# Performance work log

Measured on AMD Instinct MI355X. Metric: run time of the kernel, lower is better.

## Reference

```python
import jax, jax.numpy as jnp
import numpy as np

B, N, F, E = 4, 256, 128, 128
HID = 128      # link ConvLSTM hidden channels
L_PROP = 2     # propagate_layers
SUB, AFF = 10, 12


def setup_inputs() -> dict:
    key = jax.random.key(0)
    ks = jax.random.split(key, 16)
    s = 0.02
    inp = dict(
        edge_features=jax.random.normal(ks[0], (B, E, N, N), jnp.float32),
        node_features=jax.random.normal(ks[1], (B, F, N), jnp.float32),
        adj_mat=jax.random.uniform(ks[2], (B, N, N), dtype=jnp.float32),
        node_labels=jnp.zeros((B, N, AFF), jnp.float32),
        args=0,
    )
    # GraphConvLSTM link function: two 1x1-conv LSTM cells + 1x1 output conv
    inp['W_lstm0'] = s * jax.random.normal(ks[3], (4 * HID, E + HID), jnp.float32)
    inp['b_lstm0'] = jnp.zeros((4 * HID,), jnp.float32)
    inp['W_lstm1'] = s * jax.random.normal(ks[4], (4 * HID, HID + HID), jnp.float32)
    inp['b_lstm1'] = jnp.zeros((4 * HID,), jnp.float32)
    inp['W_link_out'] = s * jax.random.normal(ks[5], (1, HID), jnp.float32)
    inp['b_link_out'] = jnp.zeros((1,), jnp.float32)
    # linear_concat message: Linear(2F+E -> E)
    inp['W_msg'] = s * jax.random.normal(ks[6], (E, 2 * F + E), jnp.float32)
    inp['b_msg'] = jnp.zeros((E,), jnp.float32)
    # two GRU update functions (node 0 vs other nodes), input E, hidden F
    inp['Wih0'] = s * jax.random.normal(ks[7], (3 * F, E), jnp.float32)
    inp['Whh0'] = s * jax.random.normal(ks[8], (3 * F, F), jnp.float32)
    inp['bih0'] = jnp.zeros((3 * F,), jnp.float32)
    inp['bhh0'] = jnp.zeros((3 * F,), jnp.float32)
    inp['Wih1'] = s * jax.random.normal(ks[9], (3 * F, E), jnp.float32)
    inp['Whh1'] = s * jax.random.normal(ks[10], (3 * F, F), jnp.float32)
    inp['bih1'] = jnp.zeros((3 * F,), jnp.float32)
    inp['bhh1'] = jnp.zeros((3 * F,), jnp.float32)
    # fc_soft_max readouts
    inp['Wr0'] = s * jax.random.normal(ks[11], (SUB, F), jnp.float32)
    inp['br0'] = jnp.zeros((SUB,), jnp.float32)
    inp['Wr1'] = s * jax.random.normal(ks[12], (AFF, F), jnp.float32)
    inp['br1'] = jnp.zeros((AFF,), jnp.float32)
    return inp


def _link_fun(he, Ws, bs, Wo, bo):
    # he: [B, C, N, N] edge states -> predicted soft adjacency [B, N, N]
    x = he
    for W, b in zip(Ws, bs):
        hid = W.shape[0] // 4
        h0 = jnp.zeros(x.shape[:1] + (hid,) + x.shape[2:], x.dtype)
        xc = jnp.concatenate([x, h0], axis=1)
        g = jnp.einsum('oc,bcvw->bovw', W, xc) + b[None, :, None, None]
        i_g, f_g, g_g, o_g = jnp.split(g, 4, axis=1)
        c = jax.nn.sigmoid(i_g) * jnp.tanh(g_g)  # forget*c0 vanishes (c0=0)
        x = jax.nn.sigmoid(o_g) * jnp.tanh(c)
    a = jnp.einsum('oc,bcvw->bovw', Wo, x) + bo[None, :, None, None]
    return jax.nn.sigmoid(a)[:, 0]  # [B, N, N]


def _messages(node_features, edge_features, A, W_msg, b_msg):
    # X[b,:,w,i] = concat(h_i, h_w, e[i,w]); m[b,o,w,i] = (W_msg X + b) * A[b,i,w]
    hv = jnp.broadcast_to(node_features[:, :, None, :], (B, F, N, N))
    hw = jnp.broadcast_to(node_features[:, :, :, None], (B, F, N, N))
    ev = jnp.swapaxes(edge_features, 2, 3)
    X = jnp.concatenate([hv, hw, ev], axis=1)  # [B, 2F+E, N, N]
    m = jnp.einsum('of,bfwi->bowi', W_msg, X) + b_msg[None, :, None, None]
    return m * jnp.swapaxes(A, 1, 2)[:, None, :, :]


def _gru(x, h, Wih, Whh, bih, bhh):
    gi = x @ Wih.T + bih
    gh = h @ Whh.T + bhh
    ir, iz, inn = jnp.split(gi, 3, axis=-1)
    hr, hz, hn = jnp.split(gh, 3, axis=-1)
    r = jax.nn.sigmoid(ir + hr)
    z = jax.nn.sigmoid(iz + hz)
    n = jnp.tanh(inn + r * hn)
    return (1.0 - z) * n + z * h


def reference(edge_features, node_features, adj_mat, node_labels, args,
              W_lstm0, b_lstm0, W_lstm1, b_lstm1, W_link_out, b_link_out,
              W_msg, b_msg, Wih0, Whh0, bih0, bhh0, Wih1, Whh1, bih1, bhh1,
              Wr0, br0, Wr1, br1):
    he = edge_features  # hidden_edge_states[0]
    A = None
    m_sum = None
    for _ in range(L_PROP):
        A = _link_fun(he, [W_lstm0, W_lstm1], [b_lstm0, b_lstm1], W_link_out, b_link_out)
        m = _messages(node_features, edge_features, A, W_msg, b_msg)
        he = m                     # hidden_edge_states[r+1][:,:,:,i] = m_v
        m_sum = m.sum(axis=2)      # [B, E, N]: sum over source nodes w
    # GRU update (hidden node states are never rewritten in the source, so
    # only the last round's update feeds the readout)
    h = jnp.swapaxes(node_features, 1, 2)  # [B, N, F]
    x = jnp.swapaxes(m_sum, 1, 2)          # [B, N, E]
    h_new0 = _gru(x[:, :1], h[:, :1], Wih0, Whh0, bih0, bhh0)  # node 0
    h_new1 = _gru(x[:, 1:], h[:, 1:], Wih1, Whh1, bih1, bhh1)  # other nodes
    out0 = jax.nn.log_softmax(h_new0[:, 0] @ Wr0.T + br0, axis=-1)  # [B, SUB]
    out1 = jax.nn.log_softmax(h_new1 @ Wr1.T + br1, axis=-1)        # [B, N-1, AFF]
    pred = jnp.zeros(node_labels.shape, node_labels.dtype)
    pred = pred.at[:, 0, :SUB].set(out0)
    pred = pred.at[:, 1:, :].set(out1)
    return A, pred
```

## Files before the change

kernel.cpp:

```cpp
#include <hip/hip_runtime.h>

#define CH 128
#define PIXTOT (4*256*256)
#define L2E 1.4426950408889634f

typedef unsigned short u16;
typedef short short8 __attribute__((ext_vector_type(8)));
typedef float f32x4 __attribute__((ext_vector_type(4)));

__device__ __forceinline__ float bf2f(u16 u){ return __uint_as_float(((unsigned)u)<<16); }
__device__ __forceinline__ u16 f2bf(float f){
  return (u16)((__float_as_uint(f) + 0x8000u) >> 16);
}
__device__ __forceinline__ float fexp2(float x){ return __builtin_amdgcn_exp2f(x); }
__device__ __forceinline__ float frcp(float x){ return __builtin_amdgcn_rcpf(x); }
__device__ __forceinline__ float sigm(float x){ return frcp(1.f + fexp2(-L2E*x)); }
__device__ __forceinline__ float tanh_f(float x){ return 1.f - 2.f*frcp(fexp2(2.f*L2E*x)+1.f); }

__global__ __launch_bounds__(256) void wcvt_kernel(
    const float* __restrict__ W0, const float* __restrict__ bl0,
    const float* __restrict__ W1, const float* __restrict__ bl1,
    const float* __restrict__ Wm,
    u16* __restrict__ W0c, u16* __restrict__ W1c,
    float* __restrict__ b0c, float* __restrict__ b1c,
    u16* __restrict__ Wmc)
{
  int idx = blockIdx.x*256 + threadIdx.x;
  int row = idx >> 7, col = idx & 127;
  int slot = row >> 7;
  int src = (row < 128) ? row : row + 128;
  float s = (slot == 1) ? (2.f*L2E) : (-L2E);
  W0c[idx] = f2bf(W0[(size_t)src*256 + col] * s);
  W1c[idx] = f2bf(W1[(size_t)src*256 + col] * s);
  if (idx < 16384)
    Wmc[idx] = f2bf(Wm[(size_t)(idx>>7)*384 + 256 + (idx&127)]);
  if (idx < 384){
    b0c[idx] = bl0[src] * s;
    b1c[idx] = bl1[src] * s;
  }
}

__global__ __launch_bounds__(128) void uv_kernel(
    const float* __restrict__ nf, const float* __restrict__ Wmsg,
    const float* __restrict__ bmsg, float* __restrict__ U, float* __restrict__ V)
{
  int blk = blockIdx.x; int b = blk >> 8; int i = blk & 255;
  __shared__ float xs[128];
  int t = threadIdx.x;
  xs[t] = nf[((size_t)(b*CH + t))*256 + i];
  __syncthreads();
  float su = bmsg[t];
  float sv = 0.f;
  const float* w1 = Wmsg + (size_t)t*384;
  const float* w2 = w1 + 128;
  for (int f=0; f<128; f++){ float xf = xs[f]; su += w1[f]*xf; sv += w2[f]*xf; }
  U[((size_t)(b*256 + i))*CH + t] = su;
  V[((size_t)(b*256 + i))*CH + t] = sv;
}

__device__ __forceinline__ void stage_edge(
    const float* __restrict__ edge, int b, int q1, int w0, u16 (*xs)[136], int t)
{
  const int c = t >> 1, ph = (t & 1) * 32;
  const float* src = edge + ((size_t)(b*CH + c)*256 + q1)*256 + w0 + ph;
  #pragma unroll
  for (int j=0; j<8; j++){
    f32x4 v = *(const f32x4*)(src + j*4);
    u16* dst = &xs[ph + j*4][c];
    dst[0*136]=f2bf(v[0]); dst[1*136]=f2bf(v[1]);
    dst[2*136]=f2bf(v[2]); dst[3*136]=f2bf(v[3]);
  }
}

template<bool LAST>
__device__ __forceinline__ void lstm_layer(
    const u16 (*xin)[136], u16 (*xout)[136],
    const u16* __restrict__ W, const float* __restrict__ Bc,
    int oc0, int lm, int quad, const float woc[2][4], float* partial)
{
  f32x4 acc[3][2][4];
  #pragma unroll
  for (int g=0; g<3; g++)
    #pragma unroll
    for (int rs=0; rs<2; rs++)
      #pragma unroll
      for (int nt=0; nt<4; nt++){ f32x4 z = {0.f,0.f,0.f,0.f}; acc[g][rs][nt] = z; }
  #pragma unroll
  for (int k0=0; k0<128; k0+=32){
    short8 bfr[4];
    #pragma unroll
    for (int nt=0; nt<4; nt++)
      bfr[nt] = *(const short8*)&xin[nt*16+lm][k0 + quad*8];
    #pragma unroll
    for (int g=0; g<3; g++){
      #pragma unroll
      for (int rs=0; rs<2; rs++){
        const short8 afr = *(const short8*)(W + ((size_t)(g*128 + oc0 + rs*16 + lm))*128 + k0 + quad*8);
        #pragma unroll
        for (int nt=0; nt<4; nt++)
          acc[g][rs][nt] = __builtin_amdgcn_mfma_f32_16x16x32_bf16(afr, bfr[nt], acc[g][rs][nt], 0, 0, 0);
      }
    }
  }
  #pragma unroll
  for (int rs=0; rs<2; rs++){
    float bi[3][4];
    #pragma unroll
    for (int g=0; g<3; g++)
      #pragma unroll
      for (int r=0; r<4; r++) bi[g][r] = Bc[g*128 + oc0 + rs*16 + quad*4 + r];
    #pragma unroll
    for (int nt=0; nt<4; nt++){
      ushort4 w4;
      #pragma unroll
      for (int r=0; r<4; r++){
        float iv = acc[0][rs][nt][r] + bi[0][r];
        float gv = fminf(acc[1][rs][nt][r] + bi[1][r], 80.f);
        float ov = acc[2][rs][nt][r] + bi[2][r];
        float a  = fexp2(iv);
        float bb = fexp2(gv);
        float f  = fexp2(ov);
        float c  = (bb - 1.f) * frcp((1.f + a) * (bb + 1.f));
        float c2 = c*c, c4 = c2*c2;
        float p  = __builtin_fmaf(c2, 105.f, 945.f) + c4;
        float q  = __builtin_fmaf(c4, 15.f, __builtin_fmaf(c2, 420.f, 945.f));
        float xo = c * p * frcp(q * (1.f + f));
        if (LAST) partial[nt] = __builtin_fmaf(xo, woc[rs][r], partial[nt]);
        else      ((u16*)&w4)[r] = f2bf(xo);
      }
      if (!LAST)
        *(ushort4*)&xout[nt*16+lm][oc0 + rs*16 + quad*4] = w4;
    }
  }
}

template<int MODE>
__global__ __launch_bounds__(256, 2) void link_kernel(
    const float* __restrict__ edge, const float* __restrict__ A1,
    const float* __restrict__ U, const float* __restrict__ V,
    const u16* __restrict__ Wmc,
    const u16* __restrict__ W0c, const float* __restrict__ B0c,
    const u16* __restrict__ W1c, const float* __restrict__ B1c,
    const float* __restrict__ Wo, const float* __restrict__ Bo,
    float* __restrict__ Aout, float* __restrict__ outA, float* __restrict__ A2nat)
{
  __shared__ u16 xs[64][136];
  __shared__ u16 ys[64][136];
  __shared__ float red[64][17];
  const int t = threadIdx.x;
  const int Q0 = blockIdx.x * 64;
  const int b = Q0 >> 16, q1 = (Q0 >> 8) & 255, w0 = Q0 & 255;
  stage_edge(edge, b, q1, w0, xs, t);
  const int wv = t >> 6, lane = t & 63, lm = lane & 15, quad = lane >> 4;
  const int oc0 = wv*32;
  float woc[2][4];
  #pragma unroll
  for (int rs=0; rs<2; rs++){
    const f32x4 wv4 = *(const f32x4*)(Wo + oc0 + rs*16 + quad*4);
    #pragma unroll
    for (int r=0; r<4; r++) woc[rs][r] = wv4[r];
  }
  __syncthreads();
  if (MODE){
    f32x4 acc[2][4];
    #pragma unroll
    for (int rs=0; rs<2; rs++)
      #pragma unroll
      for (int nt=0; nt<4; nt++){ f32x4 z = {0.f,0.f,0.f,0.f}; acc[rs][nt] = z; }
    #pragma unroll
    for (int k0=0; k0<128; k0+=32){
      short8 bfr[4];
      #pragma unroll
      for (int nt=0; nt<4; nt++)
        bfr[nt] = *(const short8*)&xs[nt*16+lm][k0 + quad*8];
      #pragma unroll
      for (int rs=0; rs<2; rs++){
        const short8 afr = *(const short8*)(Wmc + ((size_t)(oc0 + rs*16 + lm))*128 + k0 + quad*8);
        #pragma unroll
        for (int nt=0; nt<4; nt++)
          acc[rs][nt] = __builtin_amdgcn_mfma_f32_16x16x32_bf16(afr, bfr[nt], acc[rs][nt], 0, 0, 0);
      }
    }
    #pragma unroll
    for (int rs=0; rs<2; rs++){
      const int o0 = oc0 + rs*16 + quad*4;
      const f32x4 ug = *(const f32x4*)(U + ((size_t)(b*256 + q1))*CH + o0);
      #pragma unroll
      for (int nt=0; nt<4; nt++){
        const int px = nt*16 + lm;
        const float a1 = A1[Q0 + px];
        const f32x4 vg = *(const f32x4*)(V + ((size_t)(b*256 + w0 + px))*CH + o0);
        ushort4 w4;
        #pragma unroll
        for (int r=0; r<4; r++)
          ((u16*)&w4)[r] = f2bf((acc[rs][nt][r] + ug[r] + vg[r]) * a1);
        *(ushort4*)&ys[px][o0] = w4;
      }
    }
    __syncthreads();
  }
  const u16 (*in0)[136] = MODE ? (const u16(*)[136])ys : (const u16(*)[136])xs;
  u16 (*buf)[136] = MODE ? xs : ys;
  float partial[4] = {0.f, 0.f, 0.f, 0.f};
  lstm_layer<false>(in0, buf, W0c, B0c, oc0, lm, quad, woc, partial);
  __syncthreads();
  lstm_layer<true>((const u16(*)[136])buf, (u16(*)[136])nullptr, W1c, B1c, oc0, lm, quad, woc, partial);
  #pragma unroll
  for (int nt=0; nt<4; nt++) red[nt*16+lm][wv*4+quad] = partial[nt];
  __syncthreads();
  if (t < 64){
    float s = Bo[0];
    #pragma unroll
    for (int k=0; k<16; k++) s += red[t][k];
    const float sg = sigm(s);
    Aout[Q0 + t] = sg;
    if (MODE){
      const size_t p = (size_t)b*65536 + (size_t)(w0 + t)*256 + q1;
      outA[p]  = sg;
      A2nat[p] = sg;
    }
  }
}

__global__ __launch_bounds__(256) void se_kernel(
    const float* __restrict__ edge, const float* __restrict__ A2nat,
    float* __restrict__ s_e, float* __restrict__ sA)
{
  const int b = blockIdx.x >> 8, i = blockIdx.x & 255;
  __shared__ float al[256];
  __shared__ float sb[2][128];
  __shared__ float rr[64];
  const int t = threadIdx.x;
  al[t] = A2nat[((size_t)(b*256 + i))*256 + t];
  __syncthreads();
  const int c = t & 127, half = t >> 7;
  const float* src = edge + (((size_t)(b*CH + c))*256 + i)*256 + half*128;
  float s = 0.f;
  #pragma unroll
  for (int j=0; j<32; j++){
    const f32x4 v = *(const f32x4*)(src + j*4);
    const float* ap = &al[half*128 + j*4];
    s += v[0]*ap[0] + v[1]*ap[1] + v[2]*ap[2] + v[3]*ap[3];
  }
  sb[half][c] = s;
  if (t < 64) rr[t] = al[t] + al[t+64] + al[t+128] + al[t+192];
  __syncthreads();
  if (t < 128) s_e[((size_t)(b*256 + i))*CH + t] = sb[0][t] + sb[1][t];
  if (t == 0){
    float sa = 0.f;
    for (int k=0; k<64; k++) sa += rr[k];
    sA[b*256 + i] = sa;
  }
}

__global__ __launch_bounds__(128) void mfinal_kernel(
    const float* __restrict__ s_e, const float* __restrict__ sA,
    const float* __restrict__ A2nat, const float* __restrict__ V,
    const float* __restrict__ Wmsg, const float* __restrict__ U,
    float* __restrict__ msum)
{
  const int b = blockIdx.x >> 8, i = blockIdx.x & 255;
  __shared__ float se_s[128];
  __shared__ float al[256];
  const int t = threadIdx.x;
  se_s[t] = s_e[((size_t)(b*256 + i))*CH + t];
  al[t]       = A2nat[((size_t)(b*256 + i))*256 + t];
  al[t + 128] = A2nat[((size_t)(b*256 + i))*256 + t + 128];
  __syncthreads();
  const float* w3 = Wmsg + (size_t)t*384 + 256;
  float s = U[((size_t)(b*256 + i))*CH + t] * sA[b*256 + i];
  #pragma unroll 4
  for (int k=0; k<128; k+=4){
    const f32x4 wv4 = *(const f32x4*)(w3 + k);
    s += wv4[0]*se_s[k] + wv4[1]*se_s[k+1] + wv4[2]*se_s[k+2] + wv4[3]*se_s[k+3];
  }
  const float* vp = V + ((size_t)(b*256))*CH + t;
  #pragma unroll 8
  for (int w=0; w<256; w++)
    s += al[w] * vp[(size_t)w*CH];
  msum[((size_t)(b*256 + i))*CH + t] = s;
}

__global__ __launch_bounds__(128) void k5_kernel(
    const float* __restrict__ msum, const float* __restrict__ nf,
    const float* __restrict__ Wih0, const float* __restrict__ Whh0,
    const float* __restrict__ bih0, const float* __restrict__ bhh0,
    const float* __restrict__ Wih1, const float* __restrict__ Whh1,
    const float* __restrict__ bih1, const float* __restrict__ bhh1,
    const float* __restrict__ Wr0, const float* __restrict__ br0,
    const float* __restrict__ Wr1, const float* __restrict__ br1,
    float* __restrict__ outp)
{
  const int blk = blockIdx.x, b = blk >> 8, n = blk & 255;
  __shared__ float xsh[128], hsh[128], hnew[128], lg[16];
  const int t = threadIdx.x;
  xsh[t] = msum[((size_t)(b*256 + n))*CH + t];
  hsh[t] = nf[((size_t)(b*CH + t))*256 + n];
  __syncthreads();
  const float* Wih = n ? Wih1 : Wih0;  const float* Whh = n ? Whh1 : Whh0;
  const float* bih = n ? bih1 : bih0;  const float* bhh = n ? bhh1 : bhh0;
  float gi[3], gh[3];
  #pragma unroll
  for (int prt=0; prt<3; prt++){
    int row = prt*128 + t;
    const float* wi_ = Wih + (size_t)row*CH;
    const float* wh_ = Whh + (size_t)row*CH;
    float si = 0.f, sh2 = 0.f;
    for (int k=0; k<128; k+=4){
      f32x4 wv1 = *(const f32x4*)(wi_ + k);
      f32x4 wv2 = *(const f32x4*)(wh_ + k);
      #pragma unroll
      for (int j=0; j<4; j++){ si += wv1[j]*xsh[k+j]; sh2 += wv2[j]*hsh[k+j]; }
    }
    gi[prt] = si + bih[row];
    gh[prt] = sh2 + bhh[row];
  }
  float r  = sigm(gi[0] + gh[0]);
  float z  = sigm(gi[1] + gh[1]);
  float ng = tanh_f(gi[2] + r*gh[2]);
  hnew[t] = (1.f - z)*ng + z*hsh[t];
  __syncthreads();
  const int K = n ? 12 : 10;
  const float* Wr = n ? Wr1 : Wr0;  const float* br = n ? br1 : br0;
  if (t < K){
    const float* wr_ = Wr + (size_t)t*CH;
    float s = 0.f;
    for (int k=0; k<128; k+=4){
      f32x4 wv1 = *(const f32x4*)(wr_ + k);
      #pragma unroll
      for (int j=0; j<4; j++) s += wv1[j]*hnew[k+j];
    }
    lg[t] = s + br[t];
  }
  __syncthreads();
  if (t < 12){
    float o = 0.f;
    if (t < K){
      float mx = -1e30f;
      for (int j=0; j<K; j++) mx = fmaxf(mx, lg[j]);
      float se = 0.f;
      for (int j=0; j<K; j++) se += __expf(lg[j] - mx);
      o = lg[t] - mx - __logf(se);
    }
    outp[((size_t)(b*256 + n))*12 + t] = o;
  }
}

extern "C" void kernel_launch(void* const* d_in, const int* in_sizes, int n_in,
                              void* d_out, int out_size, void* d_ws, size_t ws_size,
                              hipStream_t stream)
{
  (void)in_sizes; (void)n_in; (void)out_size; (void)ws_size;
  const float* edge = (const float*)d_in[0];
  const float* nf   = (const float*)d_in[1];
  const float* Wl0  = (const float*)d_in[5];
  const float* bl0  = (const float*)d_in[6];
  const float* Wl1  = (const float*)d_in[7];
  const float* bl1  = (const float*)d_in[8];
  const float* Wlo  = (const float*)d_in[9];
  const float* blo  = (const float*)d_in[10];
  const float* Wmsg = (const float*)d_in[11];
  const float* bmsg = (const float*)d_in[12];
  const float* Wih0 = (const float*)d_in[13];
  const float* Whh0 = (const float*)d_in[14];
  const float* bih0 = (const float*)d_in[15];
  const float* bhh0 = (const float*)d_in[16];
  const float* Wih1 = (const float*)d_in[17];
  const float* Whh1 = (const float*)d_in[18];
  const float* bih1 = (const float*)d_in[19];
  const float* bhh1 = (const float*)d_in[20];
  const float* Wr0  = (const float*)d_in[21];
  const float* br0  = (const float*)d_in[22];
  const float* Wr1  = (const float*)d_in[23];
  const float* br1  = (const float*)d_in[24];

  char* ws = (char*)d_ws;
  float* A1v   = (float*)(ws);
  float* A2nat = (float*)(ws + 1048576);
  float* U     = (float*)(ws + 2097152);
  float* V     = (float*)(ws + 2621440);
  float* msum  = (float*)(ws + 3145728);
  float* s_e   = (float*)(ws + 3670016);
  float* sAr   = (float*)(ws + 4194304);
  u16*   W0c   = (u16*)(ws + 4198400);
  u16*   W1c   = (u16*)(ws + 4296704);
  u16*   Wmc   = (u16*)(ws + 4395008);
  float* b0c   = (float*)(ws + 4427776);
  float* b1c   = (float*)(ws + 4429312);

  float* outA = (float*)d_out;
  float* outP = outA + (size_t)PIXTOT;

  wcvt_kernel<<<dim3(192), dim3(256), 0, stream>>>(
      Wl0, bl0, Wl1, bl1, Wmsg, W0c, W1c, b0c, b1c, Wmc);
  uv_kernel<<<dim3(4*256), dim3(128), 0, stream>>>(nf, Wmsg, bmsg, U, V);
  link_kernel<0><<<dim3(PIXTOT/64), dim3(256), 0, stream>>>(
      edge, (const float*)nullptr, U, V, Wmc, W0c, b0c, W1c, b1c, Wlo, blo,
      A1v, (float*)nullptr, (float*)nullptr);
  link_kernel<1><<<dim3(PIXTOT/64), dim3(256), 0, stream>>>(
      edge, A1v, U, V, Wmc, W0c, b0c, W1c, b1c, Wlo, blo,
      A1v, outA, A2nat);
  se_kernel<<<dim3(4*256), dim3(256), 0, stream>>>(edge, A2nat, s_e, sAr);
  mfinal_kernel<<<dim3(4*256), dim3(128), 0, stream>>>(
      s_e, sAr, A2nat, V, Wmsg, U, msum);
  k5_kernel<<<dim3(4*256), dim3(128), 0, stream>>>(
      msum, nf, Wih0, Whh0, bih0, bhh0, Wih1, Whh1, bih1, bhh1,
      Wr0, br0, Wr1, br1, outP);
}
```

Measured before the change: 639.2 us.

## Restructure LSTM gate loop for lower registers, MFMA-ize UV and GRU GEMMs

The LSTM layer now computes one gate at a time and keeps intermediate gate products packed as bf16 in registers. This cuts accumulator register pressure, and the launch bound is raised to 4 blocks per CU to get more occupancy. The UV projection and the GRU input/hidden GEMMs for the non-zero nodes move from scalar fp32 loops to bf16 MFMA kernels, and a new gg kernel precomputes the gate matrix G that k5b reads. The cost is extra bf16 rounding of the intermediate gate values and of the GRU inputs, and G reuses the A1 workspace region.

```diff
diff --git a/kernel.cpp b/kernel.cpp
--- a/kernel.cpp
+++ b/kernel.cpp
@@ -11,58 +11,66 @@
 __device__ __forceinline__ float bf2f(u16 u){ return __uint_as_float(((unsigned)u)<<16); }
 __device__ __forceinline__ u16 f2bf(float f){
   return (u16)((__float_as_uint(f) + 0x8000u) >> 16);
+}
+__device__ __forceinline__ unsigned pk2(float a, float b){
+  return (unsigned)f2bf(a) | ((unsigned)f2bf(b) << 16);
 }
 __device__ __forceinline__ float fexp2(float x){ return __builtin_amdgcn_exp2f(x); }
 __device__ __forceinline__ float frcp(float x){ return __builtin_amdgcn_rcpf(x); }
 __device__ __forceinline__ float sigm(float x){ return frcp(1.f + fexp2(-L2E*x)); }
 __device__ __forceinline__ float tanh_f(float x){ return 1.f - 2.f*frcp(fexp2(2.f*L2E*x)+1.f); }
+__device__ __forceinline__ float pade_tanh(float c){
+  float c2 = c*c, c4 = c2*c2;
+  float p  = __builtin_fmaf(c2, 105.f, 945.f) + c4;
+  float q  = __builtin_fmaf(c4, 15.f, __builtin_fmaf(c2, 420.f, 945.f));
+  return c * p * frcp(q);
+}
 
 __global__ __launch_bounds__(256) void wcvt_kernel(
     const float* __restrict__ W0, const float* __restrict__ bl0,
     const float* __restrict__ W1, const float* __restrict__ bl1,
     const float* __restrict__ Wm,
+    const float* __restrict__ Wih1, const float* __restrict__ Whh1,
     u16* __restrict__ W0c, u16* __restrict__ W1c,
     float* __restrict__ b0c, float* __restrict__ b1c,
-    u16* __restrict__ Wmc)
+    u16* __restrict__ Wmc, u16* __restrict__ Wuv, u16* __restrict__ Wg1)
 {
   int idx = blockIdx.x*256 + threadIdx.x;
-  int row = idx >> 7, col = idx & 127;
-  int slot = row >> 7;
-  int src = (row < 128) ? row : row + 128;
-  float s = (slot == 1) ? (2.f*L2E) : (-L2E);
-  W0c[idx] = f2bf(W0[(size_t)src*256 + col] * s);
-  W1c[idx] = f2bf(W1[(size_t)src*256 + col] * s);
+  int col = idx & 127;
+  if (idx < 49152){
+    int row = idx >> 7;
+    int slot = row >> 7;
+    int src = (row < 128) ? row : row + 128;
+    float s = (slot == 1) ? (2.f*L2E) : (-L2E);
+    W0c[idx] = f2bf(W0[(size_t)src*256 + col] * s);
+    W1c[idx] = f2bf(W1[(size_t)src*256 + col] * s);
+  }
   if (idx < 16384)
-    Wmc[idx] = f2bf(Wm[(size_t)(idx>>7)*384 + 256 + (idx&127)]);
+    Wmc[idx] = f2bf(Wm[(size_t)(idx>>7)*384 + 256 + col]);
+  if (idx < 32768){
+    int row = idx >> 7;
+    Wuv[idx] = (row < 128) ? f2bf(Wm[(size_t)row*384 + col])
+                           : f2bf(Wm[(size_t)(row-128)*384 + 128 + col]);
+  }
+  {
+    int row = idx >> 7;
+    Wg1[idx] = (row < 384) ? f2bf(Wih1[(size_t)row*128 + col])
+                           : f2bf(Whh1[(size_t)(row-384)*128 + col]);
+  }
   if (idx < 384){
+    int row = idx;
+    int src = (row < 128) ? row : row + 128;
+    float s = ((row>>7) == 1) ? (2.f*L2E) : (-L2E);
     b0c[idx] = bl0[src] * s;
     b1c[idx] = bl1[src] * s;
   }
 }
 
-__global__ __launch_bounds__(128) void uv_kernel(
-    const float* __restrict__ nf, const float* __restrict__ Wmsg,
-    const float* __restrict__ bmsg, float* __restrict__ U, float* __restrict__ V)
-{
-  int blk = blockIdx.x; int b = blk >> 8; int i = blk & 255;
-  __shared__ float xs[128];
-  int t = threadIdx.x;
-  xs[t] = nf[((size_t)(b*CH + t))*256 + i];
-  __syncthreads();
-  float su = bmsg[t];
-  float sv = 0.f;
-  const float* w1 = Wmsg + (size_t)t*384;
-  const float* w2 = w1 + 128;
-  for (int f=0; f<128; f++){ float xf = xs[f]; su += w1[f]*xf; sv += w2[f]*xf; }
-  U[((size_t)(b*256 + i))*CH + t] = su;
-  V[((size_t)(b*256 + i))*CH + t] = sv;
-}
-
-__device__ __forceinline__ void stage_edge(
-    const float* __restrict__ edge, int b, int q1, int w0, u16 (*xs)[136], int t)
+__device__ __forceinline__ void stage_cmaj(
+    const float* __restrict__ base, u16 (*xs)[136], int t)
 {
   const int c = t >> 1, ph = (t & 1) * 32;
-  const float* src = edge + ((size_t)(b*CH + c)*256 + q1)*256 + w0 + ph;
+  const float* src = base + (size_t)c*256 + ph;
   #pragma unroll
   for (int j=0; j<8; j++){
     f32x4 v = *(const f32x4*)(src + j*4);
@@ -72,70 +80,134 @@
   }
 }
 
+__global__ __launch_bounds__(256) void uvmfma_kernel(
+    const float* __restrict__ nf, const u16* __restrict__ Wuv,
+    const float* __restrict__ bmsg, float* __restrict__ U, float* __restrict__ V)
+{
+  const int b = blockIdx.x >> 2, i0 = (blockIdx.x & 3) * 64;
+  __shared__ u16 xs[64][136];
+  const int t = threadIdx.x;
+  stage_cmaj(nf + (size_t)b*CH*256 + i0, xs, t);
+  __syncthreads();
+  const int wv = t >> 6, lane = t & 63, lm = lane & 15, quad = lane >> 4;
+  f32x4 acc[4][4];
+  #pragma unroll
+  for (int rs=0; rs<4; rs++)
+    #pragma unroll
+    for (int nt=0; nt<4; nt++){ f32x4 z={0.f,0.f,0.f,0.f}; acc[rs][nt]=z; }
+  #pragma unroll
+  for (int k0=0; k0<128; k0+=32){
+    short8 bfr[4];
+    #pragma unroll
+    for (int nt=0; nt<4; nt++)
+      bfr[nt] = *(const short8*)&xs[nt*16+lm][k0 + quad*8];
+    #pragma unroll
+    for (int rs=0; rs<4; rs++){
+      const short8 afr = *(const short8*)(Wuv + ((size_t)(wv*64 + rs*16 + lm))*128 + k0 + quad*8);
+      #pragma unroll
+      for (int nt=0; nt<4; nt++)
+        acc[rs][nt] = __builtin_amdgcn_mfma_f32_16x16x32_bf16(afr, bfr[nt], acc[rs][nt], 0,0,0);
+    }
+  }
+  #pragma unroll
+  for (int rs=0; rs<4; rs++){
+    const int row0 = wv*64 + rs*16 + quad*4;
+    #pragma unroll
+    for (int nt=0; nt<4; nt++){
+      const int i = i0 + nt*16 + lm;
+      #pragma unroll
+      for (int r=0; r<4; r++){
+        const int row = row0 + r;
+        if (row < 128) U[((size_t)(b*256 + i))*CH + row] = acc[rs][nt][r] + bmsg[row];
+        else           V[((size_t)(b*256 + i))*CH + row - 128] = acc[rs][nt][r];
+      }
+    }
+  }
+}
+
 template<bool LAST>
 __device__ __forceinline__ void lstm_layer(
     const u16 (*xin)[136], u16 (*xout)[136],
     const u16* __restrict__ W, const float* __restrict__ Bc,
     int oc0, int lm, int quad, const float woc[2][4], float* partial)
 {
-  f32x4 acc[3][2][4];
-  #pragma unroll
-  for (int g=0; g<3; g++)
+  unsigned tp[2][4][2];
+  #pragma unroll
+  for (int g=0; g<3; g++){
+    f32x4 acc[2][4];
     #pragma unroll
     for (int rs=0; rs<2; rs++)
       #pragma unroll
-      for (int nt=0; nt<4; nt++){ f32x4 z = {0.f,0.f,0.f,0.f}; acc[g][rs][nt] = z; }
-  #pragma unroll
-  for (int k0=0; k0<128; k0+=32){
-    short8 bfr[4];
-    #pragma unroll
-    for (int nt=0; nt<4; nt++)
-      bfr[nt] = *(const short8*)&xin[nt*16+lm][k0 + quad*8];
-    #pragma unroll
-    for (int g=0; g<3; g++){
+      for (int nt=0; nt<4; nt++){ f32x4 z={0.f,0.f,0.f,0.f}; acc[rs][nt]=z; }
+    #pragma unroll
+    for (int k0=0; k0<128; k0+=32){
+      short8 bfr[4];
+      #pragma unroll
+      for (int nt=0; nt<4; nt++)
+        bfr[nt] = *(const short8*)&xin[nt*16+lm][k0 + quad*8];
       #pragma unroll
       for (int rs=0; rs<2; rs++){
         const short8 afr = *(const short8*)(W + ((size_t)(g*128 + oc0 + rs*16 + lm))*128 + k0 + quad*8);
         #pragma unroll
         for (int nt=0; nt<4; nt++)
-          acc[g][rs][nt] = __builtin_amdgcn_mfma_f32_16x16x32_bf16(afr, bfr[nt], acc[g][rs][nt], 0, 0, 0);
-      }
-    }
-  }
-  #pragma unroll
-  for (int rs=0; rs<2; rs++){
-    float bi[3][4];
-    #pragma unroll
-    for (int g=0; g<3; g++)
-      #pragma unroll
-      for (int r=0; r<4; r++) bi[g][r] = Bc[g*128 + oc0 + rs*16 + quad*4 + r];
-    #pragma unroll
-    for (int nt=0; nt<4; nt++){
-      ushort4 w4;
-      #pragma unroll
-      for (int r=0; r<4; r++){
-        float iv = acc[0][rs][nt][r] + bi[0][r];
-        float gv = fminf(acc[1][rs][nt][r] + bi[1][r], 80.f);
-        float ov = acc[2][rs][nt][r] + bi[2][r];
-        float a  = fexp2(iv);
-        float bb = fexp2(gv);
-        float f  = fexp2(ov);
-        float c  = (bb - 1.f) * frcp((1.f + a) * (bb + 1.f));
-        float c2 = c*c, c4 = c2*c2;
-        float p  = __builtin_fmaf(c2, 105.f, 945.f) + c4;
-        float q  = __builtin_fmaf(c4, 15.f, __builtin_fmaf(c2, 420.f, 945.f));
-        float xo = c * p * frcp(q * (1.f + f));
-        if (LAST) partial[nt] = __builtin_fmaf(xo, woc[rs][r], partial[nt]);
-        else      ((u16*)&w4)[r] = f2bf(xo);
-      }
-      if (!LAST)
-        *(ushort4*)&xout[nt*16+lm][oc0 + rs*16 + quad*4] = w4;
+          acc[rs][nt] = __builtin_amdgcn_mfma_f32_16x16x32_bf16(afr, bfr[nt], acc[rs][nt], 0,0,0);
+      }
+    }
+    #pragma unroll
+    for (int rs=0; rs<2; rs++){
+      float bi[4];
+      #pragma unroll
+      for (int r=0; r<4; r++) bi[r] = Bc[g*128 + oc0 + rs*16 + quad*4 + r];
+      #pragma unroll
+      for (int nt=0; nt<4; nt++){
+        if (g == 0){
+          float s0 = frcp(1.f + fexp2(acc[rs][nt][0] + bi[0]));
+          float s1 = frcp(1.f + fexp2(acc[rs][nt][1] + bi[1]));
+          float s2 = frcp(1.f + fexp2(acc[rs][nt][2] + bi[2]));
+          float s3 = frcp(1.f + fexp2(acc[rs][nt][3] + bi[3]));
+          tp[rs][nt][0] = pk2(s0, s1);
+          tp[rs][nt][1] = pk2(s2, s3);
+        } else if (g == 1){
+          #pragma unroll
+          for (int pr=0; pr<2; pr++){
+            float t1a = bf2f((u16)tp[rs][nt][pr]);
+            float t1b = bf2f((u16)(tp[rs][nt][pr] >> 16));
+            float ga = fminf(acc[rs][nt][pr*2]   + bi[pr*2],   80.f);
+            float gb = fminf(acc[rs][nt][pr*2+1] + bi[pr*2+1], 80.f);
+            float ea = fexp2(ga), eb = fexp2(gb);
+            float ca = t1a * (ea - 1.f) * frcp(ea + 1.f);
+            float cb = t1b * (eb - 1.f) * frcp(eb + 1.f);
+            tp[rs][nt][pr] = pk2(pade_tanh(ca), pade_tanh(cb));
+          }
+        } else {
+          float xo[4];
+          #pragma unroll
+          for (int pr=0; pr<2; pr++){
+            float tca = bf2f((u16)tp[rs][nt][pr]);
+            float tcb = bf2f((u16)(tp[rs][nt][pr] >> 16));
+            float fa = fexp2(acc[rs][nt][pr*2]   + bi[pr*2]);
+            float fb = fexp2(acc[rs][nt][pr*2+1] + bi[pr*2+1]);
+            xo[pr*2]   = tca * frcp(1.f + fa);
+            xo[pr*2+1] = tcb * frcp(1.f + fb);
+          }
+          if (LAST){
+            #pragma unroll
+            for (int r=0; r<4; r++)
+              partial[nt] = __builtin_fmaf(xo[r], woc[rs][r], partial[nt]);
+          } else {
+            ushort4 w4;
+            #pragma unroll
+            for (int r=0; r<4; r++) ((u16*)&w4)[r] = f2bf(xo[r]);
+            *(ushort4*)&xout[nt*16+lm][oc0 + rs*16 + quad*4] = w4;
+          }
+        }
+      }
     }
   }
 }
 
 template<int MODE>
-__global__ __launch_bounds__(256, 2) void link_kernel(
+__global__ __launch_bounds__(256, 4) void link_kernel(
     const float* __restrict__ edge, const float* __restrict__ A1,
     const float* __restrict__ U, const float* __restrict__ V,
     const u16* __restrict__ Wmc,
@@ -150,7 +222,7 @@
   const int t = threadIdx.x;
   const int Q0 = blockIdx.x * 64;
   const int b = Q0 >> 16, q1 = (Q0 >> 8) & 255, w0 = Q0 & 255;
-  stage_edge(edge, b, q1, w0, xs, t);
+  stage_cmaj(edge + ((size_t)b*CH*256 + q1)*256 + w0, xs, t);
   const int wv = t >> 6, lane = t & 63, lm = lane & 15, quad = lane >> 4;
   const int oc0 = wv*32;
   float woc[2][4];
@@ -166,7 +238,7 @@
     #pragma unroll
     for (int rs=0; rs<2; rs++)
       #pragma unroll
-      for (int nt=0; nt<4; nt++){ f32x4 z = {0.f,0.f,0.f,0.f}; acc[rs][nt] = z; }
+      for (int nt=0; nt<4; nt++){ f32x4 z={0.f,0.f,0.f,0.f}; acc[rs][nt]=z; }
     #pragma unroll
     for (int k0=0; k0<128; k0+=32){
       short8 bfr[4];
@@ -178,7 +250,7 @@
         const short8 afr = *(const short8*)(Wmc + ((size_t)(oc0 + rs*16 + lm))*128 + k0 + quad*8);
         #pragma unroll
         for (int nt=0; nt<4; nt++)
-          acc[rs][nt] = __builtin_amdgcn_mfma_f32_16x16x32_bf16(afr, bfr[nt], acc[rs][nt], 0, 0, 0);
+          acc[rs][nt] = __builtin_amdgcn_mfma_f32_16x16x32_bf16(afr, bfr[nt], acc[rs][nt], 0,0,0);
       }
     }
     #pragma unroll
@@ -281,39 +353,101 @@
   msum[((size_t)(b*256 + i))*CH + t] = s;
 }
 
-__global__ __launch_bounds__(128) void k5_kernel(
+__global__ __launch_bounds__(256) void gg_kernel(
     const float* __restrict__ msum, const float* __restrict__ nf,
+    const u16* __restrict__ Wg1, float* __restrict__ G)
+{
+  const int b = blockIdx.x >> 2, n0 = (blockIdx.x & 3) * 64;
+  __shared__ u16 xs[64][136];
+  __shared__ u16 hs[64][136];
+  const int t = threadIdx.x;
+  {
+    const int p = t >> 2, seg = (t & 3) * 32;
+    const float* src = msum + ((size_t)(b*256 + n0 + p))*CH + seg;
+    #pragma unroll
+    for (int j=0; j<8; j++){
+      f32x4 v = *(const f32x4*)(src + j*4);
+      xs[p][seg+j*4+0]=f2bf(v[0]); xs[p][seg+j*4+1]=f2bf(v[1]);
+      xs[p][seg+j*4+2]=f2bf(v[2]); xs[p][seg+j*4+3]=f2bf(v[3]);
+    }
+  }
+  stage_cmaj(nf + (size_t)b*CH*256 + n0, hs, t);
+  __syncthreads();
+  const int wv = t >> 6, lane = t & 63, lm = lane & 15, quad = lane >> 4;
+  #pragma unroll
+  for (int half=0; half<2; half++){
+    const u16 (*in)[136] = half ? (const u16(*)[136])hs : (const u16(*)[136])xs;
+    const u16* Wb = Wg1 + (size_t)half*384*128;
+    #pragma unroll
+    for (int rs=0; rs<6; rs++){
+      f32x4 acc[4];
+      #pragma unroll
+      for (int nt=0; nt<4; nt++){ f32x4 z={0.f,0.f,0.f,0.f}; acc[nt]=z; }
+      #pragma unroll
+      for (int k0=0; k0<128; k0+=32){
+        short8 bfr[4];
+        #pragma unroll
+        for (int nt=0; nt<4; nt++)
+          bfr[nt] = *(const short8*)&in[nt*16+lm][k0 + quad*8];
+        const short8 afr = *(const short8*)(Wb + ((size_t)(wv*96 + rs*16 + lm))*128 + k0 + quad*8);
+        #pragma unroll
+        for (int nt=0; nt<4; nt++)
+          acc[nt] = __builtin_amdgcn_mfma_f32_16x16x32_bf16(afr, bfr[nt], acc[nt], 0,0,0);
+      }
+      #pragma unroll
+      for (int nt=0; nt<4; nt++){
+        const int n = n0 + nt*16 + lm;
+        #pragma unroll
+        for (int r=0; r<4; r++)
+          G[((size_t)(b*256 + n))*768 + half*384 + wv*96 + rs*16 + quad*4 + r] = acc[nt][r];
+      }
+    }
+  }
+}
+
+__global__ __launch_bounds__(128) void k5b_kernel(
+    const float* __restrict__ G, const float* __restrict__ msum,
+    const float* __restrict__ nf,
     const float* __restrict__ Wih0, const float* __restrict__ Whh0,
     const float* __restrict__ bih0, const float* __restrict__ bhh0,
-    const float* __restrict__ Wih1, const float* __restrict__ Whh1,
     const float* __restrict__ bih1, const float* __restrict__ bhh1,
     const float* __restrict__ Wr0, const float* __restrict__ br0,
     const float* __restrict__ Wr1, const float* __restrict__ br1,
     float* __restrict__ outp)
 {
   const int blk = blockIdx.x, b = blk >> 8, n = blk & 255;
+  __shared__ float gl[768];
   __shared__ float xsh[128], hsh[128], hnew[128], lg[16];
   const int t = threadIdx.x;
-  xsh[t] = msum[((size_t)(b*256 + n))*CH + t];
   hsh[t] = nf[((size_t)(b*CH + t))*256 + n];
-  __syncthreads();
-  const float* Wih = n ? Wih1 : Wih0;  const float* Whh = n ? Whh1 : Whh0;
-  const float* bih = n ? bih1 : bih0;  const float* bhh = n ? bhh1 : bhh0;
   float gi[3], gh[3];
-  #pragma unroll
-  for (int prt=0; prt<3; prt++){
-    int row = prt*128 + t;
-    const float* wi_ = Wih + (size_t)row*CH;
-    const float* wh_ = Whh + (size_t)row*CH;
-    float si = 0.f, sh2 = 0.f;
-    for (int k=0; k<128; k+=4){
-      f32x4 wv1 = *(const f32x4*)(wi_ + k);
-      f32x4 wv2 = *(const f32x4*)(wh_ + k);
-      #pragma unroll
-      for (int j=0; j<4; j++){ si += wv1[j]*xsh[k+j]; sh2 += wv2[j]*hsh[k+j]; }
-    }
-    gi[prt] = si + bih[row];
-    gh[prt] = sh2 + bhh[row];
+  if (n == 0){
+    xsh[t] = msum[((size_t)(b*256 + n))*CH + t];
+    __syncthreads();
+    #pragma unroll
+    for (int prt=0; prt<3; prt++){
+      int row = prt*128 + t;
+      const float* wi_ = Wih0 + (size_t)row*CH;
+      const float* wh_ = Whh0 + (size_t)row*CH;
+      float si = 0.f, sh2 = 0.f;
+      for (int k=0; k<128; k+=4){
+        f32x4 wv1 = *(const f32x4*)(wi_ + k);
+        f32x4 wv2 = *(const f32x4*)(wh_ + k);
+        #pragma unroll
+        for (int j=0; j<4; j++){ si += wv1[j]*xsh[k+j]; sh2 += wv2[j]*hsh[k+j]; }
+      }
+      gi[prt] = si + bih0[row];
+      gh[prt] = sh2 + bhh0[row];
+    }
+  } else {
+    #pragma unroll
+    for (int p=0; p<6; p++) gl[p*128 + t] = G[((size_t)(b*256 + n))*768 + p*128 + t];
+    __syncthreads();
+    #pragma unroll
+    for (int prt=0; prt<3; prt++){
+      gi[prt] = gl[prt*128 + t] + bih1[prt*128 + t];
+      gh[prt] = gl[384 + prt*128 + t] + bhh1[prt*128 + t];
+    }
   }
   float r  = sigm(gi[0] + gh[0]);
   float z  = sigm(gi[1] + gh[1]);
@@ -387,13 +521,17 @@
   u16*   Wmc   = (u16*)(ws + 4395008);
   float* b0c   = (float*)(ws + 4427776);
   float* b1c   = (float*)(ws + 4429312);
+  u16*   Wuv   = (u16*)(ws + 4430848);
+  u16*   Wg1   = (u16*)(ws + 4496384);
+  float* G     = (float*)(ws);
 
   float* outA = (float*)d_out;
   float* outP = outA + (size_t)PIXTOT;
 
-  wcvt_kernel<<<dim3(192), dim3(256), 0, stream>>>(
-      Wl0, bl0, Wl1, bl1, Wmsg, W0c, W1c, b0c, b1c, Wmc);
-  uv_kernel<<<dim3(4*256), dim3(128), 0, stream>>>(nf, Wmsg, bmsg, U, V);
+  wcvt_kernel<<<dim3(384), dim3(256), 0, stream>>>(
+      Wl0, bl0, Wl1, bl1, Wmsg, Wih1, Whh1,
+      W0c, W1c, b0c, b1c, Wmc, Wuv, Wg1);
+  uvmfma_kernel<<<dim3(16), dim3(256), 0, stream>>>(nf, Wuv, bmsg, U, V);
   link_kernel<0><<<dim3(PIXTOT/64), dim3(256), 0, stream>>>(
       edge, (const float*)nullptr, U, V, Wmc, W0c, b0c, W1c, b1c, Wlo, blo,
       A1v, (float*)nullptr, (float*)nullptr);
@@ -403,7 +541,8 @@
   se_kernel<<<dim3(4*256), dim3(256), 0, stream>>>(edge, A2nat, s_e, sAr);
   mfinal_kernel<<<dim3(4*256), dim3(128), 0, stream>>>(
       s_e, sAr, A2nat, V, Wmsg, U, msum);
-  k5_kernel<<<dim3(4*256), dim3(128), 0, stream>>>(
-      msum, nf, Wih0, Whh0, bih0, bhh0, Wih1, Whh1, bih1, bhh1,
+  gg_kernel<<<dim3(16), dim3(256), 0, stream>>>(msum, nf, Wg1, G);
+  k5b_kernel<<<dim3(4*256), dim3(128), 0, stream>>>(
+      G, msum, nf, Wih0, Whh0, bih0, bhh0, bih1, bhh1,
       Wr0, br0, Wr1, br1, outP);
 }
```

Result: slower. 801.5 us (+25.4%).
